# Kernel tuning notes

Hardware: AMD Instinct MI355X
Metric: run time of the kernel (lower is better)

The kernel has to match this reference:

```python
import jax, jax.numpy as jnp
import numpy as np

B, N, D, H = 1, 4096, 512, 8
HD = D // H


def setup_inputs() -> dict:
    key = jax.random.key(0)
    ks = jax.random.split(key, 12)
    s = 0.02  # weight init scale for numerical stability
    query = jax.random.normal(ks[0], (B, N, D), jnp.float32)
    key_t = jax.random.normal(ks[1], (B, N, D), jnp.float32)
    value = jax.random.normal(ks[2], (B, N, D), jnp.float32)
    Wq = jax.random.normal(ks[3], (D, D), jnp.float32) * s
    bq = jax.random.normal(ks[4], (D,), jnp.float32) * s
    Wk = jax.random.normal(ks[5], (D, D), jnp.float32) * s
    bk = jax.random.normal(ks[6], (D,), jnp.float32) * s
    Wv = jax.random.normal(ks[7], (D, D), jnp.float32) * s
    bv = jax.random.normal(ks[8], (D,), jnp.float32) * s
    Wo = jax.random.normal(ks[9], (D, D), jnp.float32) * s
    bo = jax.random.normal(ks[10], (D,), jnp.float32) * s
    # build sgconv_mat exactly as __init__: shifted nonneg adjacency, max-normalized,
    # then symmetric degree normalization D^-1/2 A D^-1/2 (gwmha_layer_num=1)
    A = jax.random.uniform(ks[11], (N, N), jnp.float32)
    A = A + A.min()
    A = A / A.max()
    deg = A.sum(1)
    dinv = 1.0 / jnp.sqrt(deg)
    sgconv_mat = (dinv[:, None] * A * dinv[None, :])[None]  # [1,N,N]
    return {"query": query, "key": key_t, "value": value,
            "Wq": Wq, "bq": bq, "Wk": Wk, "bk": bk, "Wv": Wv, "bv": bv,
            "Wo": Wo, "bo": bo, "sgconv_mat": sgconv_mat}


def reference(query, key, value, Wq, bq, Wk, bk, Wv, bv, Wo, bo, sgconv_mat):
    b, n, d = query.shape
    q = (query @ Wq.T + bq).reshape(b, n, H, HD)
    k = (key @ Wk.T + bk).reshape(b, n, H, HD)
    v = (value @ Wv.T + bv).reshape(b, n, H, HD)
    energy = jnp.einsum('bqhd,bkhd->bhqk', q, k)
    attn = jax.nn.softmax(energy / jnp.sqrt(jnp.float32(d)), axis=3)
    out = jnp.einsum('bhqk,bkhd->bqhd', attn, v).reshape(b, n, d)
    out = sgconv_mat @ out          # [1,N,N] @ [B,N,D] -> [B,N,D]
    return out @ Wo.T + bo
```

## Files before the change

### kernel.cpp

```cpp
#include <hip/hip_runtime.h>
#include <hip/hip_bf16.h>
#include <math.h>

typedef __bf16 bf16_t;
typedef __bf16 bf16x8 __attribute__((ext_vector_type(8)));
typedef __bf16 bf16x2 __attribute__((ext_vector_type(2)));
typedef unsigned short ushort8v __attribute__((ext_vector_type(8)));
typedef float floatx4 __attribute__((ext_vector_type(4)));

static __device__ inline unsigned short f2bf_rne(float f) {
    unsigned int u = __builtin_bit_cast(unsigned int, f);
    unsigned int r = u + 0x7FFFu + ((u >> 16) & 1u);
    return (unsigned short)(r >> 16);
}
static __device__ inline bf16_t f2bf(float f) {
    return __builtin_bit_cast(bf16_t, f2bf_rne(f));
}

#if __has_builtin(__builtin_amdgcn_cvt_pk_bf16_f32)
static __device__ inline unsigned pk2bf(float a, float b) {
    bf16x2 v = __builtin_amdgcn_cvt_pk_bf16_f32(a, b);
    return __builtin_bit_cast(unsigned, v);
}
#else
static __device__ inline unsigned pk2bf(float a, float b) {
    return (unsigned)f2bf_rne(a) | ((unsigned)f2bf_rne(b) << 16);
}
#endif

#if __has_builtin(__builtin_amdgcn_exp2f)
#define EXP2F __builtin_amdgcn_exp2f
#else
#define EXP2F exp2f
#endif

static __device__ inline bf16x8 load8(const bf16_t* p) { return *(const bf16x8*)p; }
static __device__ inline bf16x8 load8(const float* p) {
    float4 a = *(const float4*)p;
    float4 b = *(const float4*)(p + 4);
    ushort8v u;
    u[0] = f2bf_rne(a.x); u[1] = f2bf_rne(a.y); u[2] = f2bf_rne(a.z); u[3] = f2bf_rne(a.w);
    u[4] = f2bf_rne(b.x); u[5] = f2bf_rne(b.y); u[6] = f2bf_rne(b.z); u[7] = f2bf_rne(b.w);
    return __builtin_bit_cast(bf16x8, u);
}
static __device__ inline bf16x8 load8sum4(const float* p, size_t s) {
    float4 a0 = *(const float4*)p,           a1 = *(const float4*)(p + 4);
    float4 b0 = *(const float4*)(p + s),     b1 = *(const float4*)(p + s + 4);
    float4 c0 = *(const float4*)(p + 2 * s), c1 = *(const float4*)(p + 2 * s + 4);
    float4 d0 = *(const float4*)(p + 3 * s), d1 = *(const float4*)(p + 3 * s + 4);
    ushort8v u;
    u[0] = f2bf_rne((a0.x + b0.x) + (c0.x + d0.x));
    u[1] = f2bf_rne((a0.y + b0.y) + (c0.y + d0.y));
    u[2] = f2bf_rne((a0.z + b0.z) + (c0.z + d0.z));
    u[3] = f2bf_rne((a0.w + b0.w) + (c0.w + d0.w));
    u[4] = f2bf_rne((a1.x + b1.x) + (c1.x + d1.x));
    u[5] = f2bf_rne((a1.y + b1.y) + (c1.y + d1.y));
    u[6] = f2bf_rne((a1.z + b1.z) + (c1.z + d1.z));
    u[7] = f2bf_rne((a1.w + b1.w) + (c1.w + d1.w));
    return __builtin_bit_cast(bf16x8, u);
}

static __device__ inline void store_c(float* C, size_t i, float v) { C[i] = v; }
static __device__ inline void store_c(bf16_t* C, size_t i, float v) { C[i] = f2bf(v); }

template <int AMODE, typename TA, typename TB, typename TC>
__device__ inline void gemm_body(
    const TA* __restrict__ A, size_t astride, int lda,
    const TB* __restrict__ B, int ldb,
    const float* __restrict__ bias_col, const float* __restrict__ bias_row,
    TC* __restrict__ C, int ldc, int K, int m0, int n0)
{
    __shared__ bf16_t As[128 * 68];
    __shared__ bf16_t Bs[64 * 68];

    const int tid = threadIdx.x;
    const int lane = tid & 63, wave = tid >> 6;
    const int wm = wave & 1, wn = wave >> 1;
    const int lo16 = lane & 15, quad = lane >> 4;
    const int sr = tid >> 2, sc = (tid & 3) * 8;

    floatx4 acc[4][2] = {};

    for (int k0 = 0; k0 < K; k0 += 32) {
        bf16x8 a0, a1, b0;
        const size_t ia0 = (size_t)(m0 + sr) * lda + k0 + sc;
        const size_t ia1 = (size_t)(m0 + 64 + sr) * lda + k0 + sc;
        if (AMODE == 1) {
            a0 = load8sum4((const float*)A + ia0, astride);
            a1 = load8sum4((const float*)A + ia1, astride);
        } else {
            a0 = load8(A + ia0);
            a1 = load8(A + ia1);
        }
        b0 = load8(B + (size_t)(n0 + sr) * ldb + k0 + sc);
        __syncthreads();
        *(bf16x8*)(&As[sr * 68 + sc]) = a0;
        *(bf16x8*)(&As[(64 + sr) * 68 + sc]) = a1;
        *(bf16x8*)(&Bs[sr * 68 + sc]) = b0;
        __syncthreads();

        bf16x8 af[4], bfv[2];
#pragma unroll
        for (int mt = 0; mt < 4; ++mt)
            af[mt] = *(const bf16x8*)(&As[(wm * 64 + mt * 16 + lo16) * 68 + quad * 8]);
#pragma unroll
        for (int nt = 0; nt < 2; ++nt)
            bfv[nt] = *(const bf16x8*)(&Bs[(wn * 32 + nt * 16 + lo16) * 68 + quad * 8]);
#pragma unroll
        for (int mt = 0; mt < 4; ++mt)
#pragma unroll
            for (int nt = 0; nt < 2; ++nt)
                acc[mt][nt] = __builtin_amdgcn_mfma_f32_16x16x32_bf16(
                    af[mt], bfv[nt], acc[mt][nt], 0, 0, 0);
    }

#pragma unroll
    for (int nt = 0; nt < 2; ++nt) {
        const int gn = n0 + wn * 32 + nt * 16 + lo16;
        const float bc = bias_col ? bias_col[gn] : 0.f;
#pragma unroll
        for (int mt = 0; mt < 4; ++mt) {
#pragma unroll
            for (int r = 0; r < 4; ++r) {
                const int gm = m0 + wm * 64 + mt * 16 + quad * 4 + r;
                float v = acc[mt][nt][r] + bc;
                if (bias_row) v += bias_row[gm];
                store_c(C, (size_t)gm * ldc + gn, v);
            }
        }
    }
}

__global__ __launch_bounds__(256) void proj_qkv(
    const float* __restrict__ query, const float* __restrict__ Wq, const float* __restrict__ bq,
    const float* __restrict__ key,   const float* __restrict__ Wk, const float* __restrict__ bk,
    const float* __restrict__ Wv,    const float* __restrict__ value, const float* __restrict__ bv,
    const float* __restrict__ sg,    bf16_t* __restrict__ sgb,
    bf16_t* __restrict__ q, bf16_t* __restrict__ k, bf16_t* __restrict__ vt)
{
    const int b = blockIdx.x;
    if (b >= 768) {
        const size_t base = (size_t)(b - 768) * 65536 + threadIdx.x * 8;
#pragma unroll 4
        for (int it = 0; it < 32; ++it) {
            const size_t idx = base + (size_t)it * 2048;
            float4 a = *(const float4*)(sg + idx);
            float4 c = *(const float4*)(sg + idx + 4);
            ushort8v u;
            u[0] = f2bf_rne(a.x); u[1] = f2bf_rne(a.y); u[2] = f2bf_rne(a.z); u[3] = f2bf_rne(a.w);
            u[4] = f2bf_rne(c.x); u[5] = f2bf_rne(c.y); u[6] = f2bf_rne(c.z); u[7] = f2bf_rne(c.w);
            *(ushort8v*)(sgb + idx) = u;
        }
        return;
    }
    const float *A, *B, *bc = nullptr, *br = nullptr;
    bf16_t* C;
    int ldc = 512, m0, n0;
    if (b < 512) {
        int i = b & 255, x = i & 7, t = i >> 3;
        n0 = (t & 7) * 64;
        m0 = ((t >> 3) * 8 + x) * 128;
        if (b < 256) { A = query; B = Wq; bc = bq; C = q; }
        else         { A = key;   B = Wk; bc = bk; C = k; }
    } else {
        int i = b - 512;
        n0 = (i & 63) * 64;
        m0 = (i >> 6) * 128;
        A = Wv; B = value; br = bv; C = vt; ldc = 4096;
    }
    gemm_body<0, float, float, bf16_t>(A, 0, 512, B, 512, bc, br, C, ldc, 512, m0, n0);
}

__global__ __launch_bounds__(256) void sgconv_gemm(
    const bf16_t* __restrict__ sgb, const bf16_t* __restrict__ aot,
    float* __restrict__ part)
{
    const int i = blockIdx.x & 127;
    const int kb = blockIdx.x >> 7;
    const int ms = i & 31, ns = i >> 5;
    const int m0 = ms * 128, n0 = ns * 128;
    const int kbase = kb * 1024;

    __shared__ bf16_t As[128 * 68];
    __shared__ bf16_t Bs[128 * 68];

    const int tid = threadIdx.x;
    const int lane = tid & 63, wave = tid >> 6;
    const int wm = wave & 1, wn = wave >> 1;
    const int lo16 = lane & 15, quad = lane >> 4;
    const int sr = tid >> 1, sc = (tid & 1) * 16;

    const bf16_t* asrc = sgb + (size_t)(m0 + sr) * 4096 + kbase + sc;
    const bf16_t* bsrc = aot + (size_t)(n0 + sr) * 4096 + kbase + sc;

    floatx4 acc[4][4] = {};

    for (int k0 = 0; k0 < 1024; k0 += 32) {
        bf16x8 a0 = *(const bf16x8*)(asrc + k0);
        bf16x8 a1 = *(const bf16x8*)(asrc + k0 + 8);
        bf16x8 b0 = *(const bf16x8*)(bsrc + k0);
        bf16x8 b1 = *(const bf16x8*)(bsrc + k0 + 8);
        __syncthreads();
        *(bf16x8*)(&As[sr * 68 + sc]) = a0;
        *(bf16x8*)(&As[sr * 68 + sc + 8]) = a1;
        *(bf16x8*)(&Bs[sr * 68 + sc]) = b0;
        *(bf16x8*)(&Bs[sr * 68 + sc + 8]) = b1;
        __syncthreads();

        bf16x8 af[4], bfv[4];
#pragma unroll
        for (int mt = 0; mt < 4; ++mt)
            af[mt] = *(const bf16x8*)(&As[(wm * 64 + mt * 16 + lo16) * 68 + quad * 8]);
#pragma unroll
        for (int nt = 0; nt < 4; ++nt)
            bfv[nt] = *(const bf16x8*)(&Bs[(wn * 64 + nt * 16 + lo16) * 68 + quad * 8]);
#pragma unroll
        for (int mt = 0; mt < 4; ++mt)
#pragma unroll
            for (int nt = 0; nt < 4; ++nt)
                acc[mt][nt] = __builtin_amdgcn_mfma_f32_16x16x32_bf16(
                    af[mt], bfv[nt], acc[mt][nt], 0, 0, 0);
    }

    float* pw = part + (size_t)kb * (4096 * 512);
#pragma unroll
    for (int mt = 0; mt < 4; ++mt)
#pragma unroll
        for (int r = 0; r < 4; ++r) {
            const int gm = m0 + wm * 64 + mt * 16 + quad * 4 + r;
#pragma unroll
            for (int nt = 0; nt < 4; ++nt)
                pw[(size_t)gm * 512 + n0 + wn * 64 + nt * 16 + lo16] = acc[mt][nt][r];
        }
}

__global__ __launch_bounds__(256) void out_proj(
    const float* __restrict__ p, const float* __restrict__ Wo,
    const float* __restrict__ bo, float* __restrict__ out)
{
    const int i = blockIdx.x, x = i & 7, t = i >> 3;
    const int n0 = (t & 7) * 64, m0 = ((t >> 3) * 8 + x) * 128;
    gemm_body<1, float, float, float>(p, (size_t)4096 * 512, 512, Wo, 512,
                                      bo, nullptr, out, 512, 512, m0, n0);
}

__global__ __launch_bounds__(256, 4) void flash_attn(
    const bf16_t* __restrict__ q, const bf16_t* __restrict__ kk,
    const bf16_t* __restrict__ vt, float* __restrict__ op,
    float* __restrict__ lp, float scale2 )
{
    const int N = 4096, D = 512;
    const int h   = blockIdx.x & 7;
    const int qb  = (blockIdx.x >> 3) & 31;
    const int qtr = blockIdx.x >> 8;
    const int t0  = qtr * 1024;

    const int tid = threadIdx.x;
    const int w = tid >> 6, lane = tid & 63;
    const int lo16 = lane & 15, quad = lane >> 4;

    __shared__ bf16_t Ks[64 * 68];
    __shared__ bf16_t Vs[64 * 68];
    __shared__ bf16_t Ps[4][32 * 68];

    const bf16_t* qp = q + (size_t)(qb * 128 + w * 32 + lo16) * D + h * 64 + quad * 8;
    bf16x8 qf[2][2];
    qf[0][0] = *(const bf16x8*)qp;
    qf[0][1] = *(const bf16x8*)(qp + 32);
    qf[1][0] = *(const bf16x8*)(qp + 16 * D);
    qf[1][1] = *(const bf16x8*)(qp + 16 * D + 32);

    ushort8v onesu;
#pragma unroll
    for (int i = 0; i < 8; ++i) onesu[i] = 0x3F80;
    const bf16x8 ones = __builtin_bit_cast(bf16x8, onesu);

    const int srow = tid >> 2, sc = (tid & 3) * 16;
    const bf16_t* ksrc = kk + (size_t)(t0 + srow) * D + h * 64 + sc;
    const bf16_t* vsrc = vt + (size_t)(h * 64 + srow) * N + t0 + sc;
    bf16_t* kdst = &Ks[srow * 68 + sc];
    bf16_t* vdst = &Vs[srow * 68 + sc];

    floatx4 o[4][2] = {};
    floatx4 ol[2] = {};

    bf16x8 kr0 = *(const bf16x8*)ksrc;
    bf16x8 kr1 = *(const bf16x8*)(ksrc + 8);
    bf16x8 vr0 = *(const bf16x8*)vsrc;
    bf16x8 vr1 = *(const bf16x8*)(vsrc + 8);

    for (int it = 0; it < 16; ++it) {
        __syncthreads();
        *(bf16x8*)kdst = kr0;  *(bf16x8*)(kdst + 8) = kr1;
        *(bf16x8*)vdst = vr0;  *(bf16x8*)(vdst + 8) = vr1;
        __syncthreads();
        if (it < 15) {
            const bf16_t* kn = ksrc + (size_t)(it + 1) * 64 * D;
            const bf16_t* vn = vsrc + (it + 1) * 64;
            kr0 = *(const bf16x8*)kn;  kr1 = *(const bf16x8*)(kn + 8);
            vr0 = *(const bf16x8*)vn;  vr1 = *(const bf16x8*)(vn + 8);
        }

        floatx4 s[4][2];
#pragma unroll
        for (int tt = 0; tt < 4; ++tt) {
            bf16x8 kf0 = *(const bf16x8*)(&Ks[(tt * 16 + lo16) * 68 + quad * 8]);
            bf16x8 kf1 = *(const bf16x8*)(&Ks[(tt * 16 + lo16) * 68 + 32 + quad * 8]);
#pragma unroll
            for (int qt = 0; qt < 2; ++qt) {
                floatx4 a = {};
                a = __builtin_amdgcn_mfma_f32_16x16x32_bf16(kf0, qf[qt][0], a, 0, 0, 0);
                a = __builtin_amdgcn_mfma_f32_16x16x32_bf16(kf1, qf[qt][1], a, 0, 0, 0);
                s[tt][qt] = a;
            }
        }
#pragma unroll
        for (int tt = 0; tt < 4; ++tt)
#pragma unroll
            for (int qt = 0; qt < 2; ++qt) {
                float e0 = EXP2F(s[tt][qt][0] * scale2);
                float e1 = EXP2F(s[tt][qt][1] * scale2);
                float e2 = EXP2F(s[tt][qt][2] * scale2);
                float e3 = EXP2F(s[tt][qt][3] * scale2);
                uint2 pk;
                pk.x = pk2bf(e0, e1);
                pk.y = pk2bf(e2, e3);
                *(uint2*)(&Ps[w][(qt * 16 + lo16) * 68 + tt * 16 + quad * 4]) = pk;
            }
#pragma unroll
        for (int ks = 0; ks < 2; ++ks) {
            bf16x8 pf0 = *(const bf16x8*)(&Ps[w][lo16 * 68 + ks * 32 + quad * 8]);
            bf16x8 pf1 = *(const bf16x8*)(&Ps[w][(16 + lo16) * 68 + ks * 32 + quad * 8]);
            ol[0] = __builtin_amdgcn_mfma_f32_16x16x32_bf16(ones, pf0, ol[0], 0, 0, 0);
            ol[1] = __builtin_amdgcn_mfma_f32_16x16x32_bf16(ones, pf1, ol[1], 0, 0, 0);
#pragma unroll
            for (int t = 0; t < 4; ++t) {
                bf16x8 vf = *(const bf16x8*)(&Vs[(t * 16 + lo16) * 68 + ks * 32 + quad * 8]);
                o[t][0] = __builtin_amdgcn_mfma_f32_16x16x32_bf16(vf, pf0, o[t][0], 0, 0, 0);
                o[t][1] = __builtin_amdgcn_mfma_f32_16x16x32_bf16(vf, pf1, o[t][1], 0, 0, 0);
            }
        }
    }

    const int g = blockIdx.x & 255;
    float* opw = op + ((size_t)qtr * 256 + g) * 8192;
#pragma unroll
    for (int t = 0; t < 4; ++t)
#pragma unroll
        for (int pt = 0; pt < 2; ++pt)
#pragma unroll
            for (int r = 0; r < 4; ++r)
                opw[(t * 16 + quad * 4 + r) * 128 + w * 32 + pt * 16 + lo16] = o[t][pt][r];

    if (quad == 0) {
        float* lpw = lp + ((size_t)qtr * 256 + g) * 128;
        lpw[w * 32 + lo16] = ol[0][0];
        lpw[w * 32 + 16 + lo16] = ol[1][0];
    }
}

__global__ __launch_bounds__(256) void attn_combine(
    const float* __restrict__ op, const float* __restrict__ lp, bf16_t* __restrict__ aot)
{
    const int g = blockIdx.x;
    const int h = g & 7, qb = g >> 3;
    const int tid = threadIdx.x;
    __shared__ float ls[128];
    if (tid < 128) {
        float s = 0.f;
#pragma unroll
        for (int qtr = 0; qtr < 4; ++qtr)
            s += lp[((size_t)qtr * 256 + g) * 128 + tid];
        ls[tid] = 1.0f / s;
    }
    __syncthreads();
    const float* b0 = op + (size_t)g * 8192;
    const size_t QS = (size_t)256 * 8192;
#pragma unroll 4
    for (int i = 0; i < 32; ++i) {
        int idx = i * 256 + tid;
        float v = b0[idx] + b0[QS + idx] + b0[2 * QS + idx] + b0[3 * QS + idx];
        int dim = idx >> 7, qc = idx & 127;
        aot[(size_t)(h * 64 + dim) * 4096 + qb * 128 + qc] = f2bf(v * ls[qc]);
    }
}

extern "C" void kernel_launch(void* const* d_in, const int* in_sizes, int n_in,
                              void* d_out, int out_size, void* d_ws, size_t ws_size,
                              hipStream_t stream)
{
    const int N = 4096, D = 512;
    const float* query = (const float*)d_in[0];
    const float* key_t = (const float*)d_in[1];
    const float* value = (const float*)d_in[2];
    const float* Wq = (const float*)d_in[3];
    const float* bq = (const float*)d_in[4];
    const float* Wk = (const float*)d_in[5];
    const float* bk = (const float*)d_in[6];
    const float* Wv = (const float*)d_in[7];
    const float* bv = (const float*)d_in[8];
    const float* Wo = (const float*)d_in[9];
    const float* bo = (const float*)d_in[10];
    const float* sg = (const float*)d_in[11];
    float* out = (float*)d_out;

    bf16_t* q   = (bf16_t*)d_ws;
    bf16_t* kk  = q   + (size_t)N * D;
    bf16_t* vt  = kk  + (size_t)N * D;
    bf16_t* aot = vt  + (size_t)N * D;
    float*  op  = (float*)(aot + (size_t)N * D);
    float*  lp  = op + (size_t)4 * 256 * 8192;
    bf16_t* sgb = (bf16_t*)(lp + (size_t)4 * 256 * 128);
    float*  p   = op;

    const dim3 blk(256);

    proj_qkv<<<1024, blk, 0, stream>>>(query, Wq, bq, key_t, Wk, bk,
                                       Wv, value, bv, sg, sgb, q, kk, vt);

    const float scale2 = 1.4426950408889634f / sqrtf((float)D);
    flash_attn<<<1024, blk, 0, stream>>>(q, kk, vt, op, lp, scale2);
    attn_combine<<<256, blk, 0, stream>>>(op, lp, aot);

    sgconv_gemm<<<512, blk, 0, stream>>>(sgb, aot, p);
    out_proj<<<256, blk, 0, stream>>>(p, Wo, bo, out);

    (void)in_sizes; (void)n_in; (void)out_size; (void)ws_size;
}
```

Measured before the change: 295.4 us.

## Pre-convert inputs to bf16, split partial reduction, sum softmax denominators in registers

Adds a prep kernel that converts query/key/value and all weights to bf16 once, so the GEMM bodies load bf16 directly instead of converting fp32 tiles on the fly. The sg conversion is spread over more, smaller blocks. A separate part_reduce kernel sums the four split-K partials into bf16 before out_proj. Flash attention now accumulates the row sums in registers with shuffles instead of extra MFMAs against a ones vector. These add two kernel launches and extra bf16 round-trips through global memory.

```diff
diff --git a/kernel.cpp b/kernel.cpp
--- a/kernel.cpp
+++ b/kernel.cpp
@@ -34,39 +34,22 @@
 #define EXP2F exp2f
 #endif
 
-static __device__ inline bf16x8 load8(const bf16_t* p) { return *(const bf16x8*)p; }
-static __device__ inline bf16x8 load8(const float* p) {
-    float4 a = *(const float4*)p;
-    float4 b = *(const float4*)(p + 4);
+static __device__ inline void store_c(float* C, size_t i, float v) { C[i] = v; }
+static __device__ inline void store_c(bf16_t* C, size_t i, float v) { C[i] = f2bf(v); }
+
+static __device__ inline void cvt8(const float* src, bf16_t* dst, size_t idx) {
+    float4 a = *(const float4*)(src + idx);
+    float4 c = *(const float4*)(src + idx + 4);
     ushort8v u;
     u[0] = f2bf_rne(a.x); u[1] = f2bf_rne(a.y); u[2] = f2bf_rne(a.z); u[3] = f2bf_rne(a.w);
-    u[4] = f2bf_rne(b.x); u[5] = f2bf_rne(b.y); u[6] = f2bf_rne(b.z); u[7] = f2bf_rne(b.w);
-    return __builtin_bit_cast(bf16x8, u);
-}
-static __device__ inline bf16x8 load8sum4(const float* p, size_t s) {
-    float4 a0 = *(const float4*)p,           a1 = *(const float4*)(p + 4);
-    float4 b0 = *(const float4*)(p + s),     b1 = *(const float4*)(p + s + 4);
-    float4 c0 = *(const float4*)(p + 2 * s), c1 = *(const float4*)(p + 2 * s + 4);
-    float4 d0 = *(const float4*)(p + 3 * s), d1 = *(const float4*)(p + 3 * s + 4);
-    ushort8v u;
-    u[0] = f2bf_rne((a0.x + b0.x) + (c0.x + d0.x));
-    u[1] = f2bf_rne((a0.y + b0.y) + (c0.y + d0.y));
-    u[2] = f2bf_rne((a0.z + b0.z) + (c0.z + d0.z));
-    u[3] = f2bf_rne((a0.w + b0.w) + (c0.w + d0.w));
-    u[4] = f2bf_rne((a1.x + b1.x) + (c1.x + d1.x));
-    u[5] = f2bf_rne((a1.y + b1.y) + (c1.y + d1.y));
-    u[6] = f2bf_rne((a1.z + b1.z) + (c1.z + d1.z));
-    u[7] = f2bf_rne((a1.w + b1.w) + (c1.w + d1.w));
-    return __builtin_bit_cast(bf16x8, u);
-}
-
-static __device__ inline void store_c(float* C, size_t i, float v) { C[i] = v; }
-static __device__ inline void store_c(bf16_t* C, size_t i, float v) { C[i] = f2bf(v); }
-
-template <int AMODE, typename TA, typename TB, typename TC>
+    u[4] = f2bf_rne(c.x); u[5] = f2bf_rne(c.y); u[6] = f2bf_rne(c.z); u[7] = f2bf_rne(c.w);
+    *(ushort8v*)(dst + idx) = u;
+}
+
+template <typename TC>
 __device__ inline void gemm_body(
-    const TA* __restrict__ A, size_t astride, int lda,
-    const TB* __restrict__ B, int ldb,
+    const bf16_t* __restrict__ A, int lda,
+    const bf16_t* __restrict__ B, int ldb,
     const float* __restrict__ bias_col, const float* __restrict__ bias_row,
     TC* __restrict__ C, int ldc, int K, int m0, int n0)
 {
@@ -82,17 +65,9 @@
     floatx4 acc[4][2] = {};
 
     for (int k0 = 0; k0 < K; k0 += 32) {
-        bf16x8 a0, a1, b0;
-        const size_t ia0 = (size_t)(m0 + sr) * lda + k0 + sc;
-        const size_t ia1 = (size_t)(m0 + 64 + sr) * lda + k0 + sc;
-        if (AMODE == 1) {
-            a0 = load8sum4((const float*)A + ia0, astride);
-            a1 = load8sum4((const float*)A + ia1, astride);
-        } else {
-            a0 = load8(A + ia0);
-            a1 = load8(A + ia1);
-        }
-        b0 = load8(B + (size_t)(n0 + sr) * ldb + k0 + sc);
+        bf16x8 a0 = *(const bf16x8*)(A + (size_t)(m0 + sr) * lda + k0 + sc);
+        bf16x8 a1 = *(const bf16x8*)(A + (size_t)(m0 + 64 + sr) * lda + k0 + sc);
+        bf16x8 b0 = *(const bf16x8*)(B + (size_t)(n0 + sr) * ldb + k0 + sc);
         __syncthreads();
         *(bf16x8*)(&As[sr * 68 + sc]) = a0;
         *(bf16x8*)(&As[(64 + sr) * 68 + sc]) = a1;
@@ -131,44 +106,59 @@
     }
 }
 
+__global__ __launch_bounds__(256) void prep(
+    const float* __restrict__ query, const float* __restrict__ key, const float* __restrict__ value,
+    const float* __restrict__ Wq, const float* __restrict__ Wk,
+    const float* __restrict__ Wv, const float* __restrict__ Wo,
+    bf16_t* qB, bf16_t* kB, bf16_t* vB,
+    bf16_t* wqB, bf16_t* wkB, bf16_t* wvB, bf16_t* woB)
+{
+    const int b = blockIdx.x;
+    const float* src; bf16_t* dst; size_t base;
+    if      (b < 256) { src = query; dst = qB;  base = (size_t)b * 8192; }
+    else if (b < 512) { src = key;   dst = kB;  base = (size_t)(b - 256) * 8192; }
+    else if (b < 768) { src = value; dst = vB;  base = (size_t)(b - 512) * 8192; }
+    else if (b < 800) { src = Wq;    dst = wqB; base = (size_t)(b - 768) * 8192; }
+    else if (b < 832) { src = Wk;    dst = wkB; base = (size_t)(b - 800) * 8192; }
+    else if (b < 864) { src = Wv;    dst = wvB; base = (size_t)(b - 832) * 8192; }
+    else              { src = Wo;    dst = woB; base = (size_t)(b - 864) * 8192; }
+#pragma unroll
+    for (int it = 0; it < 4; ++it)
+        cvt8(src, dst, base + (size_t)it * 2048 + threadIdx.x * 8);
+}
+
 __global__ __launch_bounds__(256) void proj_qkv(
-    const float* __restrict__ query, const float* __restrict__ Wq, const float* __restrict__ bq,
-    const float* __restrict__ key,   const float* __restrict__ Wk, const float* __restrict__ bk,
-    const float* __restrict__ Wv,    const float* __restrict__ value, const float* __restrict__ bv,
-    const float* __restrict__ sg,    bf16_t* __restrict__ sgb,
+    const bf16_t* __restrict__ qB, const bf16_t* __restrict__ wqB, const float* __restrict__ bq,
+    const bf16_t* __restrict__ kB, const bf16_t* __restrict__ wkB, const float* __restrict__ bk,
+    const bf16_t* __restrict__ wvB, const bf16_t* __restrict__ vB, const float* __restrict__ bv,
+    const float* __restrict__ sg, bf16_t* __restrict__ sgb,
     bf16_t* __restrict__ q, bf16_t* __restrict__ k, bf16_t* __restrict__ vt)
 {
     const int b = blockIdx.x;
     if (b >= 768) {
-        const size_t base = (size_t)(b - 768) * 65536 + threadIdx.x * 8;
-#pragma unroll 4
-        for (int it = 0; it < 32; ++it) {
-            const size_t idx = base + (size_t)it * 2048;
-            float4 a = *(const float4*)(sg + idx);
-            float4 c = *(const float4*)(sg + idx + 4);
-            ushort8v u;
-            u[0] = f2bf_rne(a.x); u[1] = f2bf_rne(a.y); u[2] = f2bf_rne(a.z); u[3] = f2bf_rne(a.w);
-            u[4] = f2bf_rne(c.x); u[5] = f2bf_rne(c.y); u[6] = f2bf_rne(c.z); u[7] = f2bf_rne(c.w);
-            *(ushort8v*)(sgb + idx) = u;
-        }
+        const size_t base = (size_t)(b - 768) * 8192;
+#pragma unroll
+        for (int it = 0; it < 4; ++it)
+            cvt8(sg, sgb, base + (size_t)it * 2048 + threadIdx.x * 8);
         return;
     }
-    const float *A, *B, *bc = nullptr, *br = nullptr;
+    const bf16_t *A, *B;
+    const float *bc = nullptr, *br = nullptr;
     bf16_t* C;
     int ldc = 512, m0, n0;
     if (b < 512) {
         int i = b & 255, x = i & 7, t = i >> 3;
         n0 = (t & 7) * 64;
         m0 = ((t >> 3) * 8 + x) * 128;
-        if (b < 256) { A = query; B = Wq; bc = bq; C = q; }
-        else         { A = key;   B = Wk; bc = bk; C = k; }
+        if (b < 256) { A = qB; B = wqB; bc = bq; C = q; }
+        else         { A = kB; B = wkB; bc = bk; C = k; }
     } else {
         int i = b - 512;
         n0 = (i & 63) * 64;
         m0 = (i >> 6) * 128;
-        A = Wv; B = value; br = bv; C = vt; ldc = 4096;
-    }
-    gemm_body<0, float, float, bf16_t>(A, 0, 512, B, 512, bc, br, C, ldc, 512, m0, n0);
+        A = wvB; B = vB; br = bv; C = vt; ldc = 4096;
+    }
+    gemm_body<bf16_t>(A, 512, B, 512, bc, br, C, ldc, 512, m0, n0);
 }
 
 __global__ __launch_bounds__(256) void sgconv_gemm(
@@ -234,14 +224,35 @@
         }
 }
 
+__global__ __launch_bounds__(256) void part_reduce(
+    const float* __restrict__ p, bf16_t* __restrict__ o2)
+{
+    const size_t S = (size_t)4096 * 512;
+    const size_t idx = ((size_t)blockIdx.x * 256 + threadIdx.x) * 8;
+    ushort8v u;
+#pragma unroll
+    for (int half = 0; half < 2; ++half) {
+        float4 s = *(const float4*)(p + idx + half * 4);
+#pragma unroll
+        for (int kb = 1; kb < 4; ++kb) {
+            float4 t = *(const float4*)(p + kb * S + idx + half * 4);
+            s.x += t.x; s.y += t.y; s.z += t.z; s.w += t.w;
+        }
+        u[half * 4 + 0] = f2bf_rne(s.x);
+        u[half * 4 + 1] = f2bf_rne(s.y);
+        u[half * 4 + 2] = f2bf_rne(s.z);
+        u[half * 4 + 3] = f2bf_rne(s.w);
+    }
+    *(ushort8v*)(o2 + idx) = u;
+}
+
 __global__ __launch_bounds__(256) void out_proj(
-    const float* __restrict__ p, const float* __restrict__ Wo,
+    const bf16_t* __restrict__ o2, const bf16_t* __restrict__ woB,
     const float* __restrict__ bo, float* __restrict__ out)
 {
     const int i = blockIdx.x, x = i & 7, t = i >> 3;
     const int n0 = (t & 7) * 64, m0 = ((t >> 3) * 8 + x) * 128;
-    gemm_body<1, float, float, float>(p, (size_t)4096 * 512, 512, Wo, 512,
-                                      bo, nullptr, out, 512, 512, m0, n0);
+    gemm_body<float>(o2, 512, woB, 512, bo, nullptr, out, 512, 512, m0, n0);
 }
 
 __global__ __launch_bounds__(256, 4) void flash_attn(
@@ -270,11 +281,6 @@
     qf[1][0] = *(const bf16x8*)(qp + 16 * D);
     qf[1][1] = *(const bf16x8*)(qp + 16 * D + 32);
 
-    ushort8v onesu;
-#pragma unroll
-    for (int i = 0; i < 8; ++i) onesu[i] = 0x3F80;
-    const bf16x8 ones = __builtin_bit_cast(bf16x8, onesu);
-
     const int srow = tid >> 2, sc = (tid & 3) * 16;
     const bf16_t* ksrc = kk + (size_t)(t0 + srow) * D + h * 64 + sc;
     const bf16_t* vsrc = vt + (size_t)(h * 64 + srow) * N + t0 + sc;
@@ -282,7 +288,7 @@
     bf16_t* vdst = &Vs[srow * 68 + sc];
 
     floatx4 o[4][2] = {};
-    floatx4 ol[2] = {};
+    float l[2] = {0.f, 0.f};
 
     bf16x8 kr0 = *(const bf16x8*)ksrc;
     bf16x8 kr1 = *(const bf16x8*)(ksrc + 8);
@@ -322,6 +328,7 @@
                 float e1 = EXP2F(s[tt][qt][1] * scale2);
                 float e2 = EXP2F(s[tt][qt][2] * scale2);
                 float e3 = EXP2F(s[tt][qt][3] * scale2);
+                l[qt] += (e0 + e1) + (e2 + e3);
                 uint2 pk;
                 pk.x = pk2bf(e0, e1);
                 pk.y = pk2bf(e2, e3);
@@ -331,8 +338,6 @@
         for (int ks = 0; ks < 2; ++ks) {
             bf16x8 pf0 = *(const bf16x8*)(&Ps[w][lo16 * 68 + ks * 32 + quad * 8]);
             bf16x8 pf1 = *(const bf16x8*)(&Ps[w][(16 + lo16) * 68 + ks * 32 + quad * 8]);
-            ol[0] = __builtin_amdgcn_mfma_f32_16x16x32_bf16(ones, pf0, ol[0], 0, 0, 0);
-            ol[1] = __builtin_amdgcn_mfma_f32_16x16x32_bf16(ones, pf1, ol[1], 0, 0, 0);
 #pragma unroll
             for (int t = 0; t < 4; ++t) {
                 bf16x8 vf = *(const bf16x8*)(&Vs[(t * 16 + lo16) * 68 + ks * 32 + quad * 8]);
@@ -342,6 +347,12 @@
         }
     }
 
+#pragma unroll
+    for (int qt = 0; qt < 2; ++qt) {
+        l[qt] += __shfl_xor(l[qt], 16);
+        l[qt] += __shfl_xor(l[qt], 32);
+    }
+
     const int g = blockIdx.x & 255;
     float* opw = op + ((size_t)qtr * 256 + g) * 8192;
 #pragma unroll
@@ -354,8 +365,8 @@
 
     if (quad == 0) {
         float* lpw = lp + ((size_t)qtr * 256 + g) * 128;
-        lpw[w * 32 + lo16] = ol[0][0];
-        lpw[w * 32 + 16 + lo16] = ol[1][0];
+        lpw[w * 32 + lo16] = l[0];
+        lpw[w * 32 + 16 + lo16] = l[1];
     }
 }
 
@@ -404,26 +415,44 @@
     const float* sg = (const float*)d_in[11];
     float* out = (float*)d_out;
 
-    bf16_t* q   = (bf16_t*)d_ws;
-    bf16_t* kk  = q   + (size_t)N * D;
-    bf16_t* vt  = kk  + (size_t)N * D;
-    bf16_t* aot = vt  + (size_t)N * D;
-    float*  op  = (float*)(aot + (size_t)N * D);
-    float*  lp  = op + (size_t)4 * 256 * 8192;
-    bf16_t* sgb = (bf16_t*)(lp + (size_t)4 * 256 * 128);
-    float*  p   = op;
+    const size_t ND = (size_t)N * D;
+    const size_t DD = (size_t)D * D;
+
+    char* base = (char*)d_ws;
+    bf16_t* q    = (bf16_t*)base;
+    bf16_t* kk   = q   + ND;
+    bf16_t* vt   = kk  + ND;
+    bf16_t* aot  = vt  + ND;
+    bf16_t* sgb  = aot + ND;
+    char* regA   = (char*)(sgb + (size_t)N * N);
+    bf16_t* qB   = (bf16_t*)regA;
+    bf16_t* kB   = qB + ND;
+    bf16_t* vB   = kB + ND;
+    bf16_t* wqB  = vB + ND;
+    bf16_t* wkB  = wqB + DD;
+    bf16_t* wvB  = wkB + DD;
+    float* op    = (float*)regA;
+    float* p     = (float*)regA;
+    char* tail   = regA + (size_t)4 * 256 * 8192 * 4;
+    float*  lp   = (float*)tail;
+    bf16_t* woB  = (bf16_t*)(lp + (size_t)4 * 256 * 128);
+    bf16_t* o2   = woB + DD;
 
     const dim3 blk(256);
 
-    proj_qkv<<<1024, blk, 0, stream>>>(query, Wq, bq, key_t, Wk, bk,
-                                       Wv, value, bv, sg, sgb, q, kk, vt);
+    prep<<<896, blk, 0, stream>>>(query, key_t, value, Wq, Wk, Wv, Wo,
+                                  qB, kB, vB, wqB, wkB, wvB, woB);
+
+    proj_qkv<<<2816, blk, 0, stream>>>(qB, wqB, bq, kB, wkB, bk,
+                                       wvB, vB, bv, sg, sgb, q, kk, vt);
 
     const float scale2 = 1.4426950408889634f / sqrtf((float)D);
     flash_attn<<<1024, blk, 0, stream>>>(q, kk, vt, op, lp, scale2);
     attn_combine<<<256, blk, 0, stream>>>(op, lp, aot);
 
     sgconv_gemm<<<512, blk, 0, stream>>>(sgb, aot, p);
-    out_proj<<<256, blk, 0, stream>>>(p, Wo, bo, out);
+    part_reduce<<<1024, blk, 0, stream>>>(p, o2);
+    out_proj<<<256, blk, 0, stream>>>(o2, woB, bo, out);
 
     (void)in_sizes; (void)n_in; (void)out_size; (void)ws_size;
 }
```

New measurement: 283.9 us. -3.9%, faster.
